# Performance work log

Measured on AMD Instinct MI355X. Metric: run time of the kernel, lower is better.

Reference implementation:

```python
import jax, jax.numpy as jnp
import numpy as np

N_NODES = 30000
N_EDGES = 150000
N_REL = 10
IN_DIM = 256
OUT_DIM = 256


def setup_inputs() -> dict:
    key = jax.random.key(0)
    ks = jax.random.split(key, 10)
    s = 1.0 / np.sqrt(IN_DIM)  # ~nn.Linear init scale
    return {
        "x": jax.random.normal(ks[0], (N_NODES, IN_DIM), jnp.float32),
        "W_self": jax.random.uniform(ks[1], (IN_DIM, OUT_DIM), jnp.float32, -s, s),
        "b_self": jax.random.uniform(ks[2], (OUT_DIM,), jnp.float32, -s, s),
        "W_fwd": jax.random.uniform(ks[3], (N_REL, IN_DIM, OUT_DIM), jnp.float32, -s, s),
        "b_fwd": jax.random.uniform(ks[4], (N_REL, OUT_DIM), jnp.float32, -s, s),
        "W_rev": jax.random.uniform(ks[5], (N_REL, IN_DIM, OUT_DIM), jnp.float32, -s, s),
        "b_rev": jax.random.uniform(ks[6], (N_REL, OUT_DIM), jnp.float32, -s, s),
        "dep_idx": jax.random.randint(ks[7], (N_EDGES,), 0, N_NODES, jnp.int32),
        "rel_idx": jax.random.randint(ks[8], (N_EDGES,), 0, N_REL, jnp.int32),
        "gov_idx": jax.random.randint(ks[9], (N_EDGES,), 0, N_NODES, jnp.int32),
    }


def reference(x, W_self, b_self, W_fwd, b_fwd, W_rev, b_rev, dep_idx, rel_idx, gov_idx):
    # self transform for every token: [N, out]
    out = x @ W_self + b_self
    # transform all nodes by every relation weight up-front: [R, N, out]
    H_fwd = jnp.einsum("ni,rio->rno", x, W_fwd) + b_fwd[:, None, :]
    H_rev = jnp.einsum("ni,rio->rno", x, W_rev) + b_rev[:, None, :]
    # per-edge gather: forward msg uses governor feature, reverse msg uses dependent
    msg_fwd = H_fwd[rel_idx, gov_idx]  # [E, out]
    msg_rev = H_rev[rel_idx, dep_idx]  # [E, out]
    # scatter-add: forward msg -> dependent, reverse msg -> governor
    out = out.at[dep_idx].add(msg_fwd)
    out = out.at[gov_idx].add(msg_rev)
    return out
```

## Files before the change

### kernel.cpp

```cpp
#include <hip/hip_runtime.h>

#define N_NODES 30000
#define N_EDGES 150000
#define N_REL 10
#define DIM 256

#define SORT_BLOCKS 120
#define SORT_CHUNK ((N_EDGES + SORT_BLOCKS - 1) / SORT_BLOCKS)

#define SCAN_CHUNK 256
#define SCAN_BLOCKS ((N_NODES + SCAN_CHUNK - 1) / SCAN_CHUNK)

#define PREP_XB 7500
#define PREP_WB 5376

typedef __attribute__((ext_vector_type(8))) short bf16x8;
typedef __attribute__((ext_vector_type(4))) float f32x4;

__device__ __forceinline__ unsigned short f2bf(float f) {
  union { float f; unsigned int u; } v; v.f = f;
  unsigned int u = v.u;
  unsigned int r = u + 0x7fffu + ((u >> 16) & 1u);
  return (unsigned short)(r >> 16);
}


__global__ void prep_hist_kernel(const float* __restrict__ x,
                                 const float* __restrict__ Wf,
                                 const float* __restrict__ Wr,
                                 const float* __restrict__ Ws,
                                 const int* __restrict__ rel,
                                 const int* __restrict__ dep,
                                 const int* __restrict__ gov,
                                 unsigned short* __restrict__ xbf,
                                 unsigned short* __restrict__ wt,
                                 int* __restrict__ block_counts,
                                 int* __restrict__ cnt) {
  int b = blockIdx.x;
  if (b < PREP_XB) {
    int idx = b * 256 + threadIdx.x;
    float4 v = reinterpret_cast<const float4*>(x)[idx];
    ushort4 o;
    o.x = f2bf(v.x); o.y = f2bf(v.y); o.z = f2bf(v.z); o.w = f2bf(v.w);
    reinterpret_cast<ushort4*>(xbf)[idx] = o;
  } else if (b < PREP_XB + PREP_WB) {
    int idx = (b - PREP_XB) * 256 + threadIdx.x;
    int bb = idx >> 16;
    int t = idx & 65535;
    int o = t >> 8, i = t & 255;
    const float* src = (bb < N_REL) ? (Wf + (size_t)bb * 65536)
                     : (bb < 2 * N_REL) ? (Wr + (size_t)(bb - N_REL) * 65536)
                     : Ws;
    wt[idx] = f2bf(src[i * 256 + o]);
  } else {
    int hb = b - PREP_XB - PREP_WB;
    __shared__ int h[N_REL];
    if (threadIdx.x < N_REL) h[threadIdx.x] = 0;
    __syncthreads();
    int beg = hb * SORT_CHUNK;
    int end = min(beg + SORT_CHUNK, N_EDGES);
    for (int e = beg + threadIdx.x; e < end; e += blockDim.x) {
      atomicAdd(&h[rel[e]], 1);
      atomicAdd(&cnt[dep[e]], 1);
      atomicAdd(&cnt[N_NODES + gov[e]], 1);
    }
    __syncthreads();
    if (threadIdx.x < N_REL)
      block_counts[hb * N_REL + threadIdx.x] = h[threadIdx.x];
  }
}


__global__ void scanA_kernel(const int* __restrict__ cnt,
                             int* __restrict__ tmp, int* __restrict__ sums) {
  __shared__ int s[SCAN_CHUNK];
  int d = blockIdx.y, b = blockIdx.x, t = threadIdx.x;
  int i = b * SCAN_CHUNK + t;
  int v = (i < N_NODES) ? cnt[d * N_NODES + i] : 0;
  s[t] = v;
  __syncthreads();
  for (int off = 1; off < SCAN_CHUNK; off <<= 1) {
    int add = (t >= off) ? s[t - off] : 0;
    __syncthreads();
    s[t] += add;
    __syncthreads();
  }
  if (i < N_NODES) tmp[d * N_NODES + i] = s[t] - v;
  if (t == SCAN_CHUNK - 1) sums[d * SCAN_BLOCKS + b] = s[t];
}


__global__ void scan_finish_kernel(const int* __restrict__ sums,
                                   const int* __restrict__ tmp,
                                   const int* __restrict__ block_counts,
                                   int* __restrict__ rp,
                                   int* __restrict__ cursor,
                                   int* __restrict__ rel_start,
                                   int* __restrict__ block_offset) {
  int d = blockIdx.y, b = blockIdx.x, t = threadIdx.x;

  if (b == SCAN_BLOCKS) {
    if (d == 1) return;
    __shared__ int tot[N_REL];
    __shared__ int rstart[N_REL + 1];
    int r = t;
    if (r < N_REL) {
      int s = 0;
      for (int bb = 0; bb < SORT_BLOCKS; ++bb) s += block_counts[bb * N_REL + r];
      tot[r] = s;
    }
    __syncthreads();
    if (t == 0) {
      int s = 0;
      for (int i = 0; i < N_REL; ++i) { rstart[i] = s; s += tot[i]; }
      rstart[N_REL] = s;
      for (int i = 0; i <= N_REL; ++i) rel_start[i] = rstart[i];
    }
    __syncthreads();
    if (r < N_REL) {
      int run = rstart[r];
      for (int bb = 0; bb < SORT_BLOCKS; ++bb) {
        block_offset[bb * N_REL + r] = run;
        run += block_counts[bb * N_REL + r];
      }
    }
    return;
  }

  __shared__ int ssum[SCAN_BLOCKS];
  __shared__ int spre[SCAN_BLOCKS + 1];
  if (t < SCAN_BLOCKS) ssum[t] = sums[d * SCAN_BLOCKS + t];
  __syncthreads();
  if (t == 0) {
    int run = 0;
    for (int i = 0; i < SCAN_BLOCKS; ++i) { spre[i] = run; run += ssum[i]; }
    spre[SCAN_BLOCKS] = run;
  }
  __syncthreads();
  int chunk = spre[b];
  int i = b * SCAN_CHUNK + t;
  if (i < N_NODES) {
    int v = tmp[d * N_NODES + i] + chunk;
    rp[d * (N_NODES + 1) + i] = v;
    cursor[d * N_NODES + i] = v;
  }
  if (b == 0 && t == 0) rp[d * (N_NODES + 1) + N_NODES] = spre[SCAN_BLOCKS];
}


__global__ void scatter_all_kernel(const int* __restrict__ rel,
                                   const int* __restrict__ dep,
                                   const int* __restrict__ gov,
                                   const int* __restrict__ block_offset,
                                   int* __restrict__ cursor,
                                   int* __restrict__ perm,
                                   int* __restrict__ srcf,
                                   int* __restrict__ srcr,
                                   int* __restrict__ colf,
                                   int* __restrict__ colr) {
  __shared__ int cur[N_REL];
  if (threadIdx.x < N_REL)
    cur[threadIdx.x] = block_offset[blockIdx.x * N_REL + threadIdx.x];
  __syncthreads();
  int beg = blockIdx.x * SORT_CHUNK;
  int end = min(beg + SORT_CHUNK, N_EDGES);
  for (int e = beg + threadIdx.x; e < end; e += blockDim.x) {
    int dp = dep[e], gv = gov[e];
    int pos = atomicAdd(&cur[rel[e]], 1);
    perm[pos] = e;
    srcf[pos] = gv;
    srcr[pos] = dp;
    colf[atomicAdd(&cursor[dp], 1)] = pos;
    colr[atomicAdd(&cursor[N_NODES + gv], 1)] = pos;
  }
}


__global__ __launch_bounds__(256, 2)
void mega_gemm_kernel(const unsigned short* __restrict__ xbf,
                      const unsigned short* __restrict__ wt,
                      const float* __restrict__ b_self,
                      const float* __restrict__ b_fwd,
                      const float* __restrict__ b_rev,
                      const int* __restrict__ srcf,
                      const int* __restrict__ srcr,
                      const int* __restrict__ rel_start,
                      unsigned short* __restrict__ msg,
                      float* __restrict__ out) {
  const int bkt = blockIdx.y;
  const bool is_self = (bkt >= 2 * N_REL);
  const bool fwd = bkt < N_REL;
  const int r = is_self ? 0 : (fwd ? bkt : bkt - N_REL);

  int beg, cnt;
  const int* src_arr = fwd ? srcf : srcr;
  unsigned short* mdir = msg + (fwd ? 0 : (size_t)N_EDGES * DIM);
  if (is_self) {
    beg = (bkt - 2 * N_REL) * (N_NODES / 2);
    cnt = N_NODES / 2;
  } else {
    beg = rel_start[r];
    cnt = rel_start[r + 1] - beg;
  }
  const int ntiles = (cnt + 63) >> 6;
  const int GX = gridDim.x;

  const int tid = threadIdx.x;
  const int wave = tid >> 6, lane = tid & 63;
  const int lm = lane & 15, q = lane >> 4;
  const int nb = wave * 64;
  const int half = lane >> 5;

  __shared__ int s_src[2][64];
  __shared__ unsigned short sA[2][64 * DIM];

  bf16x8 wf[8][4];
  const unsigned short* wbase =
      wt + (size_t)(is_self ? 2 * N_REL : bkt) * DIM * DIM;
  #pragma unroll
  for (int kk = 0; kk < 8; ++kk)
    #pragma unroll
    for (int ni = 0; ni < 4; ++ni)
      wf[kk][ni] = *reinterpret_cast<const bf16x8*>(
          wbase + (size_t)(nb + ni * 16 + lm) * DIM + kk * 32 + q * 8);

  const float* bptr = is_self ? b_self : ((fwd ? b_fwd : b_rev) + r * DIM);
  float bias[4];
  #pragma unroll
  for (int ni = 0; ni < 4; ++ni) bias[ni] = bptr[nb + ni * 16 + lm];

  int swz[8];
  #pragma unroll
  for (int i = 0; i < 8; ++i)
    swz[i] = (((lane & 31) ^ ((i * 2 + half) & 7)) * 8);
  int rowoff[4];
  #pragma unroll
  for (int mi = 0; mi < 4; ++mi) rowoff[mi] = (mi * 16 + lm) * DIM;
  int ckoff[8];
  #pragma unroll
  for (int kk = 0; kk < 8; ++kk)
    ckoff[kk] = ((kk * 4 + q) ^ (lm & 7)) * 8;

  int t = blockIdx.x;
  if (t >= ntiles) return;

  auto load_idx = [&](int tt) -> int {
    int tile0_ = tt << 6;
    if (is_self) {
      int rr = beg + tile0_ + tid;
      return rr < beg + cnt ? rr : beg + cnt - 1;
    } else {
      int p_ = tile0_ + tid;
      p_ = p_ < cnt ? p_ : cnt - 1;
      return src_arr[beg + p_];
    }
  };

  auto issue_stage = [&](int p) {
    const int* sp = s_src[p];
    unsigned short* db = sA[p];
    #pragma unroll
    for (int i = 0; i < 8; ++i) {
      int ldsrow = wave * 16 + i * 2;
      int rr = sp[ldsrow + half];
      const unsigned short* g = xbf + (size_t)rr * DIM + swz[i];
      __builtin_amdgcn_global_load_lds(
          (const __attribute__((address_space(1))) void*)g,
          (__attribute__((address_space(3))) void*)(db + ldsrow * DIM),
          16, 0, 0);
    }
  };

  auto step = [&](int cur) {
    const int tile0 = t << 6;
    const int rows_valid = min(64, cnt - tile0);
    const bool have_next = (t + GX) < ntiles;
    const bool have_next2 = (t + 2 * GX) < ntiles;

    if (is_self) {
      __syncthreads();
    } else {
      asm volatile("s_waitcnt vmcnt(16) lgkmcnt(0)" ::: "memory");
      __builtin_amdgcn_s_barrier();
      __builtin_amdgcn_sched_barrier(0);
    }
    if (have_next) issue_stage(cur ^ 1);
    if (tid < 64 && have_next2) s_src[cur][tid] = load_idx(t + 2 * GX);

    const unsigned short* sAb = sA[cur];
    #pragma unroll
    for (int mi = 0; mi < 4; ++mi) {
      bf16x8 a[8];
      #pragma unroll
      for (int kk = 0; kk < 8; ++kk)
        a[kk] = *reinterpret_cast<const bf16x8*>(sAb + rowoff[mi] + ckoff[kk]);

      f32x4 acc[4];
      #pragma unroll
      for (int ni = 0; ni < 4; ++ni) acc[ni] = (f32x4){0.f, 0.f, 0.f, 0.f};

      __builtin_amdgcn_s_setprio(1);
      #pragma unroll
      for (int kk = 0; kk < 8; ++kk)
        #pragma unroll
        for (int ni = 0; ni < 4; ++ni)
          acc[ni] = __builtin_amdgcn_mfma_f32_16x16x32_bf16(
              a[kk], wf[kk][ni], acc[ni], 0, 0, 0);
      __builtin_amdgcn_s_setprio(0);

      if (is_self) {
        #pragma unroll
        for (int reg = 0; reg < 4; ++reg) {
          int row = mi * 16 + q * 4 + reg;
          if (row < rows_valid) {
            #pragma unroll
            for (int ni = 0; ni < 4; ++ni)
              out[(size_t)(beg + tile0 + row) * DIM + nb + ni * 16 + lm] =
                  acc[ni][reg] + bias[ni];
          }
        }
      } else {
        #pragma unroll
        for (int reg = 0; reg < 4; ++reg) {
          int row = mi * 16 + q * 4 + reg;
          if (row < rows_valid) {
            unsigned int p0 = ((unsigned int)f2bf(acc[1][reg] + bias[1]) << 16) |
                              f2bf(acc[0][reg] + bias[0]);
            unsigned int p1 = ((unsigned int)f2bf(acc[3][reg] + bias[3]) << 16) |
                              f2bf(acc[2][reg] + bias[2]);
            uint2 u; u.x = p0; u.y = p1;
            *reinterpret_cast<uint2*>(
                mdir + (size_t)(beg + tile0 + row) * DIM + nb + lm * 4) = u;
          }
        }
      }
    }
  };

  if (tid < 64) s_src[0][tid] = load_idx(t);
  __syncthreads();
  issue_stage(0);
  if (tid < 64 && t + GX < ntiles) s_src[1][tid] = load_idx(t + GX);
  if (!is_self)
    asm volatile("s_waitcnt vmcnt(0)" ::: "memory");

  while (true) {
    step(0);
    t += GX; if (t >= ntiles) break;
    step(1);
    t += GX; if (t >= ntiles) break;
  }
}


__global__ void reduce_both_kernel(const unsigned short* __restrict__ msg,
                                   const int* __restrict__ rp,
                                   const int* __restrict__ colf,
                                   const int* __restrict__ colr,
                                   float* __restrict__ out) {
  const int n = blockIdx.x * 4 + (threadIdx.x >> 6);
  if (n >= N_NODES) return;
  const int lane = threadIdx.x & 63;
  const int b0 = rp[n], e0 = rp[n + 1];
  const int b1 = rp[(N_NODES + 1) + n], e1 = rp[(N_NODES + 1) + n + 1];
  if (e0 == b0 && e1 == b1) return;

  float a0 = 0.f, a1 = 0.f, a2 = 0.f, a3 = 0.f;
  union { unsigned int u; float f; } c;

  auto accum = [&](unsigned long long v) {
    unsigned int lo = (unsigned int)v;
    unsigned int hi = (unsigned int)(v >> 32);
    c.u = lo << 16;          a0 += c.f;
    c.u = lo & 0xffff0000u;  a1 += c.f;
    c.u = hi << 16;          a2 += c.f;
    c.u = hi & 0xffff0000u;  a3 += c.f;
  };

  int j = b0;
  for (; j + 1 < e0; j += 2) {
    int r0 = colf[j], r1 = colf[j + 1];
    unsigned long long v0 = __builtin_nontemporal_load(
        reinterpret_cast<const unsigned long long*>(msg + (size_t)r0 * DIM + lane * 4));
    unsigned long long v1 = __builtin_nontemporal_load(
        reinterpret_cast<const unsigned long long*>(msg + (size_t)r1 * DIM + lane * 4));
    accum(v0); accum(v1);
  }
  if (j < e0) {
    unsigned long long v = __builtin_nontemporal_load(
        reinterpret_cast<const unsigned long long*>(msg + (size_t)colf[j] * DIM + lane * 4));
    accum(v);
  }
  const unsigned short* mrev = msg + (size_t)N_EDGES * DIM;
  j = b1;
  for (; j + 1 < e1; j += 2) {
    int r0 = colr[j], r1 = colr[j + 1];
    unsigned long long v0 = __builtin_nontemporal_load(
        reinterpret_cast<const unsigned long long*>(mrev + (size_t)r0 * DIM + lane * 4));
    unsigned long long v1 = __builtin_nontemporal_load(
        reinterpret_cast<const unsigned long long*>(mrev + (size_t)r1 * DIM + lane * 4));
    accum(v0); accum(v1);
  }
  if (j < e1) {
    unsigned long long v = __builtin_nontemporal_load(
        reinterpret_cast<const unsigned long long*>(mrev + (size_t)colr[j] * DIM + lane * 4));
    accum(v);
  }

  const int cb = (lane >> 4) * 64 + (lane & 15);
  float* op = out + (size_t)n * DIM;
  op[cb +  0] += a0;
  op[cb + 16] += a1;
  op[cb + 32] += a2;
  op[cb + 48] += a3;
}


__global__ __launch_bounds__(256, 2)
void self_gemm_kernel(const unsigned short* __restrict__ xbf,
                      const unsigned short* __restrict__ wt_self,
                      const float* __restrict__ b_self,
                      float* __restrict__ out) {
  const int tid = threadIdx.x;
  const int wave = tid >> 6, lane = tid & 63;
  const int lm = lane & 15, q = lane >> 4;
  const int nb = wave * 64;

  bf16x8 wf[8][4];
  #pragma unroll
  for (int kk = 0; kk < 8; ++kk)
    #pragma unroll
    for (int ni = 0; ni < 4; ++ni)
      wf[kk][ni] = *reinterpret_cast<const bf16x8*>(
          wt_self + (size_t)(nb + ni * 16 + lm) * DIM + kk * 32 + q * 8);

  float bias[4];
  #pragma unroll
  for (int ni = 0; ni < 4; ++ni) bias[ni] = b_self[nb + ni * 16 + lm];

  const int ntiles = (N_NODES + 63) / 64;
  for (int t = blockIdx.x; t < ntiles; t += gridDim.x) {
    const int row0 = t * 64;
    const unsigned short* xr[4];
    #pragma unroll
    for (int mi = 0; mi < 4; ++mi) {
      int r = row0 + mi * 16 + lm;
      int rc = r < N_NODES ? r : N_NODES - 1;
      xr[mi] = xbf + (size_t)rc * DIM + q * 8;
    }

    f32x4 acc[4][4];
    #pragma unroll
    for (int mi = 0; mi < 4; ++mi)
      #pragma unroll
      for (int ni = 0; ni < 4; ++ni)
        acc[mi][ni] = (f32x4){0.f, 0.f, 0.f, 0.f};

    #pragma unroll
    for (int kk = 0; kk < 8; ++kk) {
      bf16x8 a[4];
      #pragma unroll
      for (int mi = 0; mi < 4; ++mi)
        a[mi] = *reinterpret_cast<const bf16x8*>(xr[mi] + kk * 32);
      #pragma unroll
      for (int mi = 0; mi < 4; ++mi)
        #pragma unroll
        for (int ni = 0; ni < 4; ++ni)
          acc[mi][ni] = __builtin_amdgcn_mfma_f32_16x16x32_bf16(a[mi], wf[kk][ni], acc[mi][ni], 0, 0, 0);
    }

    #pragma unroll
    for (int mi = 0; mi < 4; ++mi) {
      #pragma unroll
      for (int reg = 0; reg < 4; ++reg) {
        int row = row0 + mi * 16 + q * 4 + reg;
        if (row < N_NODES) {
          #pragma unroll
          for (int ni = 0; ni < 4; ++ni)
            out[(size_t)row * DIM + nb + ni * 16 + lm] = acc[mi][ni][reg] + bias[ni];
        }
      }
    }
  }
}

__global__ void edge_gemm_atomic_kernel(const unsigned short* __restrict__ xbf,
                                        const unsigned short* __restrict__ wt,
                                        const float* __restrict__ b_fwd,
                                        const float* __restrict__ b_rev,
                                        const int* __restrict__ perm,
                                        const int* __restrict__ rel_start,
                                        const int* __restrict__ dep,
                                        const int* __restrict__ gov,
                                        float* __restrict__ out) {
  const int bucket = blockIdx.y;
  const int r = bucket % N_REL;
  const bool fwd = bucket < N_REL;
  const int beg = rel_start[r];
  const int cnt = rel_start[r + 1] - beg;
  const int ntiles = (cnt + 63) >> 6;

  const int tid = threadIdx.x;
  const int wave = tid >> 6, lane = tid & 63;
  const int lm = lane & 15, q = lane >> 4;
  const int nb = wave * 64;

  __shared__ int s_src[64], s_dst[64];

  const unsigned short* wr[4];
  #pragma unroll
  for (int ni = 0; ni < 4; ++ni)
    wr[ni] = wt + (size_t)bucket * DIM * DIM + (size_t)(nb + ni * 16 + lm) * DIM + q * 8;

  const float* bptr = (fwd ? b_fwd : b_rev) + r * DIM;
  float bias[4];
  #pragma unroll
  for (int ni = 0; ni < 4; ++ni) bias[ni] = bptr[nb + ni * 16 + lm];

  for (int t = blockIdx.x; t < ntiles; t += gridDim.x) {
    const int tile0 = t << 6;
    const int rows_valid = min(64, cnt - tile0);

    if (tid < 64) {
      int s = 0, d = -1;
      if (tid < rows_valid) {
        int e = perm[beg + tile0 + tid];
        int gv = gov[e], dp = dep[e];
        s = fwd ? gv : dp;
        d = fwd ? dp : gv;
      }
      s_src[tid] = s;
      s_dst[tid] = d;
    }
    __syncthreads();

    const unsigned short* xr[4];
    #pragma unroll
    for (int mi = 0; mi < 4; ++mi)
      xr[mi] = xbf + (size_t)s_src[mi * 16 + lm] * DIM + q * 8;

    f32x4 acc[4][4];
    #pragma unroll
    for (int mi = 0; mi < 4; ++mi)
      #pragma unroll
      for (int ni = 0; ni < 4; ++ni)
        acc[mi][ni] = (f32x4){0.f, 0.f, 0.f, 0.f};

    #pragma unroll
    for (int k0 = 0; k0 < DIM; k0 += 32) {
      bf16x8 a[4], b[4];
      #pragma unroll
      for (int mi = 0; mi < 4; ++mi) a[mi] = *reinterpret_cast<const bf16x8*>(xr[mi] + k0);
      #pragma unroll
      for (int ni = 0; ni < 4; ++ni) b[ni] = *reinterpret_cast<const bf16x8*>(wr[ni] + k0);
      #pragma unroll
      for (int mi = 0; mi < 4; ++mi)
        #pragma unroll
        for (int ni = 0; ni < 4; ++ni)
          acc[mi][ni] = __builtin_amdgcn_mfma_f32_16x16x32_bf16(a[mi], b[ni], acc[mi][ni], 0, 0, 0);
    }

    #pragma unroll
    for (int mi = 0; mi < 4; ++mi) {
      #pragma unroll
      for (int reg = 0; reg < 4; ++reg) {
        int row = mi * 16 + q * 4 + reg;
        if (row < rows_valid) {
          int dst = s_dst[row];
          float* op = out + (size_t)dst * DIM + nb + lm;
          #pragma unroll
          for (int ni = 0; ni < 4; ++ni)
            atomicAdd(op + ni * 16, acc[mi][ni][reg] + bias[ni]);
        }
      }
    }
    __syncthreads();
  }
}


extern "C" void kernel_launch(void* const* d_in, const int* in_sizes, int n_in,
                              void* d_out, int out_size, void* d_ws, size_t ws_size,
                              hipStream_t stream) {
  const float* x      = (const float*)d_in[0];
  const float* W_self = (const float*)d_in[1];
  const float* b_self = (const float*)d_in[2];
  const float* W_fwd  = (const float*)d_in[3];
  const float* b_fwd  = (const float*)d_in[4];
  const float* W_rev  = (const float*)d_in[5];
  const float* b_rev  = (const float*)d_in[6];
  const int* dep = (const int*)d_in[7];
  const int* rel = (const int*)d_in[8];
  const int* gov = (const int*)d_in[9];
  float* out = (float*)d_out;

  char* base = (char*)d_ws;
  size_t off = 0;
  auto alloc = [&](size_t bytes) -> char* {
    char* p = base + off;
    off = (off + bytes + 15) & ~(size_t)15;
    return p;
  };

  unsigned short* xbf = (unsigned short*)alloc((size_t)N_NODES * DIM * 2);
  unsigned short* wt  = (unsigned short*)alloc((size_t)21 * DIM * DIM * 2);
  int* perm          = (int*)alloc((size_t)N_EDGES * 4);
  int* srcf          = (int*)alloc((size_t)N_EDGES * 4);
  int* srcr          = (int*)alloc((size_t)N_EDGES * 4);
  int* rel_start     = (int*)alloc(16 * 4);
  int* block_counts  = (int*)alloc(SORT_BLOCKS * N_REL * 4);
  int* block_offset  = (int*)alloc(SORT_BLOCKS * N_REL * 4);
  int* cnt       = (int*)alloc((size_t)2 * N_NODES * 4);
  int* tmp       = (int*)alloc((size_t)2 * N_NODES * 4);
  int* sums      = (int*)alloc((size_t)2 * SCAN_BLOCKS * 4);
  int* rp        = (int*)alloc((size_t)2 * (N_NODES + 1) * 4);
  int* cursor    = (int*)alloc((size_t)2 * N_NODES * 4);
  int* colf      = (int*)alloc((size_t)N_EDGES * 4);
  int* colr      = (int*)alloc((size_t)N_EDGES * 4);
  unsigned short* msg = (unsigned short*)alloc((size_t)2 * N_EDGES * DIM * 2);
  const bool two_phase = (off <= ws_size);

  hipMemsetAsync(cnt, 0, (size_t)2 * N_NODES * 4, stream);
  prep_hist_kernel<<<PREP_XB + PREP_WB + SORT_BLOCKS, 256, 0, stream>>>(
      x, W_fwd, W_rev, W_self, rel, dep, gov, xbf, wt, block_counts, cnt);
  scanA_kernel<<<dim3(SCAN_BLOCKS, 2), SCAN_CHUNK, 0, stream>>>(cnt, tmp, sums);
  scan_finish_kernel<<<dim3(SCAN_BLOCKS + 1, 2), SCAN_CHUNK, 0, stream>>>(
      sums, tmp, block_counts, rp, cursor, rel_start, block_offset);
  scatter_all_kernel<<<SORT_BLOCKS, 256, 0, stream>>>(
      rel, dep, gov, block_offset, cursor, perm, srcf, srcr, colf, colr);

  if (two_phase) {
    mega_gemm_kernel<<<dim3(48, 2 * N_REL + 2), 256, 0, stream>>>(
        xbf, wt, b_self, b_fwd, b_rev, srcf, srcr, rel_start, msg, out);
    reduce_both_kernel<<<(N_NODES + 3) / 4, 256, 0, stream>>>(
        msg, rp, colf, colr, out);
  } else {
    self_gemm_kernel<<<120, 256, 0, stream>>>(
        xbf, wt + (size_t)20 * DIM * DIM, b_self, out);
    edge_gemm_atomic_kernel<<<dim3(260, 20), 256, 0, stream>>>(
        xbf, wt, b_fwd, b_rev, perm, rel_start, dep, gov, out);
  }
}
```

Before: 287.5 us.

## Tile weight transpose through LDS, simplify gemm sync, interleave reduce loads

The weight conversion now transposes 32x32 tiles through shared memory, so both reads and writes are coalesced, where before each thread did a strided read. In the mega gemm, the hand-tuned partial vmcnt wait plus raw barrier is replaced by a plain __syncthreads, and the initial vmcnt(0) drain is removed. The reduce kernel interleaves forward and reverse edge loads so each iteration has four gathers in flight. The sync change may serialize the async LDS prefetch more than the old partial wait did, trading some overlap for simplicity.

```diff
diff --git a/kernel.cpp b/kernel.cpp
--- a/kernel.cpp
+++ b/kernel.cpp
@@ -12,7 +12,7 @@
 #define SCAN_BLOCKS ((N_NODES + SCAN_CHUNK - 1) / SCAN_CHUNK)
 
 #define PREP_XB 7500
-#define PREP_WB 5376
+#define PREP_WT 1344
 
 typedef __attribute__((ext_vector_type(8))) short bf16x8;
 typedef __attribute__((ext_vector_type(4))) float f32x4;
@@ -43,17 +43,30 @@
     ushort4 o;
     o.x = f2bf(v.x); o.y = f2bf(v.y); o.z = f2bf(v.z); o.w = f2bf(v.w);
     reinterpret_cast<ushort4*>(xbf)[idx] = o;
-  } else if (b < PREP_XB + PREP_WB) {
-    int idx = (b - PREP_XB) * 256 + threadIdx.x;
-    int bb = idx >> 16;
-    int t = idx & 65535;
-    int o = t >> 8, i = t & 255;
+  } else if (b < PREP_XB + PREP_WT) {
+    int wb = b - PREP_XB;
+    int bb = wb >> 6;
+    int tile = wb & 63;
+    int ib = tile >> 3, ob = tile & 7;
     const float* src = (bb < N_REL) ? (Wf + (size_t)bb * 65536)
                      : (bb < 2 * N_REL) ? (Wr + (size_t)(bb - N_REL) * 65536)
                      : Ws;
-    wt[idx] = f2bf(src[i * 256 + o]);
+    __shared__ unsigned short tile_s[32][33];
+    int c = threadIdx.x & 31, r0 = threadIdx.x >> 5;
+    #pragma unroll
+    for (int k = 0; k < 4; ++k) {
+      int rr = r0 + k * 8;
+      tile_s[rr][c] = f2bf(src[(ib * 32 + rr) * 256 + ob * 32 + c]);
+    }
+    __syncthreads();
+    #pragma unroll
+    for (int k = 0; k < 4; ++k) {
+      int rr = r0 + k * 8;
+      wt[(size_t)bb * 65536 + (ob * 32 + rr) * 256 + ib * 32 + c] =
+          tile_s[c][rr];
+    }
   } else {
-    int hb = b - PREP_XB - PREP_WB;
+    int hb = b - PREP_XB - PREP_WT;
     __shared__ int h[N_REL];
     if (threadIdx.x < N_REL) h[threadIdx.x] = 0;
     __syncthreads();
@@ -277,13 +290,7 @@
     const bool have_next = (t + GX) < ntiles;
     const bool have_next2 = (t + 2 * GX) < ntiles;
 
-    if (is_self) {
-      __syncthreads();
-    } else {
-      asm volatile("s_waitcnt vmcnt(16) lgkmcnt(0)" ::: "memory");
-      __builtin_amdgcn_s_barrier();
-      __builtin_amdgcn_sched_barrier(0);
-    }
+    __syncthreads();
     if (have_next) issue_stage(cur ^ 1);
     if (tid < 64 && have_next2) s_src[cur][tid] = load_idx(t + 2 * GX);
 
@@ -341,8 +348,6 @@
   __syncthreads();
   issue_stage(0);
   if (tid < 64 && t + GX < ntiles) s_src[1][tid] = load_idx(t + GX);
-  if (!is_self)
-    asm volatile("s_waitcnt vmcnt(0)" ::: "memory");
 
   while (true) {
     step(0);
@@ -365,6 +370,7 @@
   const int b1 = rp[(N_NODES + 1) + n], e1 = rp[(N_NODES + 1) + n + 1];
   if (e0 == b0 && e1 == b1) return;
 
+  const unsigned short* mrev = msg + (size_t)N_EDGES * DIM;
   float a0 = 0.f, a1 = 0.f, a2 = 0.f, a3 = 0.f;
   union { unsigned int u; float f; } c;
 
@@ -376,36 +382,34 @@
     c.u = hi << 16;          a2 += c.f;
     c.u = hi & 0xffff0000u;  a3 += c.f;
   };
-
-  int j = b0;
-  for (; j + 1 < e0; j += 2) {
-    int r0 = colf[j], r1 = colf[j + 1];
-    unsigned long long v0 = __builtin_nontemporal_load(
-        reinterpret_cast<const unsigned long long*>(msg + (size_t)r0 * DIM + lane * 4));
-    unsigned long long v1 = __builtin_nontemporal_load(
-        reinterpret_cast<const unsigned long long*>(msg + (size_t)r1 * DIM + lane * 4));
+  auto ldf = [&](int j) -> unsigned long long {
+    return __builtin_nontemporal_load(
+        reinterpret_cast<const unsigned long long*>(
+            msg + (size_t)colf[j] * DIM + lane * 4));
+  };
+  auto ldr = [&](int j) -> unsigned long long {
+    return __builtin_nontemporal_load(
+        reinterpret_cast<const unsigned long long*>(
+            mrev + (size_t)colr[j] * DIM + lane * 4));
+  };
+
+  int j0 = b0, j1 = b1;
+  while (j0 + 1 < e0 && j1 + 1 < e1) {
+    unsigned long long v0 = ldf(j0), v1 = ldf(j0 + 1);
+    unsigned long long v2 = ldr(j1), v3 = ldr(j1 + 1);
+    accum(v0); accum(v1); accum(v2); accum(v3);
+    j0 += 2; j1 += 2;
+  }
+  for (; j0 + 1 < e0; j0 += 2) {
+    unsigned long long v0 = ldf(j0), v1 = ldf(j0 + 1);
     accum(v0); accum(v1);
   }
-  if (j < e0) {
-    unsigned long long v = __builtin_nontemporal_load(
-        reinterpret_cast<const unsigned long long*>(msg + (size_t)colf[j] * DIM + lane * 4));
-    accum(v);
-  }
-  const unsigned short* mrev = msg + (size_t)N_EDGES * DIM;
-  j = b1;
-  for (; j + 1 < e1; j += 2) {
-    int r0 = colr[j], r1 = colr[j + 1];
-    unsigned long long v0 = __builtin_nontemporal_load(
-        reinterpret_cast<const unsigned long long*>(mrev + (size_t)r0 * DIM + lane * 4));
-    unsigned long long v1 = __builtin_nontemporal_load(
-        reinterpret_cast<const unsigned long long*>(mrev + (size_t)r1 * DIM + lane * 4));
+  if (j0 < e0) accum(ldf(j0));
+  for (; j1 + 1 < e1; j1 += 2) {
+    unsigned long long v0 = ldr(j1), v1 = ldr(j1 + 1);
     accum(v0); accum(v1);
   }
-  if (j < e1) {
-    unsigned long long v = __builtin_nontemporal_load(
-        reinterpret_cast<const unsigned long long*>(mrev + (size_t)colr[j] * DIM + lane * 4));
-    accum(v);
-  }
+  if (j1 < e1) accum(ldr(j1));
 
   const int cb = (lane >> 4) * 64 + (lane & 15);
   float* op = out + (size_t)n * DIM;
@@ -621,7 +625,7 @@
   const bool two_phase = (off <= ws_size);
 
   hipMemsetAsync(cnt, 0, (size_t)2 * N_NODES * 4, stream);
-  prep_hist_kernel<<<PREP_XB + PREP_WB + SORT_BLOCKS, 256, 0, stream>>>(
+  prep_hist_kernel<<<PREP_XB + PREP_WT + SORT_BLOCKS, 256, 0, stream>>>(
       x, W_fwd, W_rev, W_self, rel, dep, gov, xbf, wt, block_counts, cnt);
   scanA_kernel<<<dim3(SCAN_BLOCKS, 2), SCAN_CHUNK, 0, stream>>>(cnt, tmp, sums);
   scan_finish_kernel<<<dim3(SCAN_BLOCKS + 1, 2), SCAN_CHUNK, 0, stream>>>(
```

Measured after the change: 279.4 us, median of 2. 1.03x faster.
